# Kernel optimization log

Measured on AMD Instinct MI355X. Metric: run time of the kernel, lower is better.

The kernel has to match this reference:

```python
import jax, jax.numpy as jnp
import numpy as np

N_NODES, N_EDGES = 50000, 800000
IN_DIM, HID, HEADS, OUT_DIM = 256, 32, 8, 16
NEG_SLOPE = 0.2  # PyG GATConv default leaky-relu slope
EPS = 1e-16      # PyG softmax denominator epsilon


def setup_inputs() -> dict:
    key = jax.random.key(0)
    ks = jax.random.split(key, 12)
    x = jax.random.normal(ks[0], (N_NODES, IN_DIM), dtype=jnp.float32)
    edge_index = jax.random.randint(ks[1], (2, N_EDGES), 0, N_NODES, dtype=jnp.int32)
    s1 = 1.0 / np.sqrt(IN_DIM)
    s2 = 1.0 / np.sqrt(HID * HEADS)
    return {
        "x": x,
        "edge_index": edge_index,
        "W1": jax.random.normal(ks[2], (IN_DIM, HEADS * HID), dtype=jnp.float32) * s1,
        "att_src1": jax.random.normal(ks[3], (HEADS, HID), dtype=jnp.float32) * s1,
        "att_dst1": jax.random.normal(ks[4], (HEADS, HID), dtype=jnp.float32) * s1,
        "bias1": jnp.zeros((HEADS * HID,), dtype=jnp.float32),
        "W2": jax.random.normal(ks[5], (HEADS * HID, HEADS * OUT_DIM), dtype=jnp.float32) * s2,
        "att_src2": jax.random.normal(ks[6], (HEADS, OUT_DIM), dtype=jnp.float32) * s2,
        "att_dst2": jax.random.normal(ks[7], (HEADS, OUT_DIM), dtype=jnp.float32) * s2,
        "bias2": jnp.zeros((OUT_DIM,), dtype=jnp.float32),
    }


def _gat_conv(x, src, dst, W, att_src, att_dst, bias, concat):
    # x: [N, F_in]; src/dst: [E'] (self-loops already appended)
    N = x.shape[0]
    H, C = att_src.shape
    h = (x @ W).reshape(N, H, C)                      # [N, H, C]
    a_src = jnp.einsum('nhc,hc->nh', h, att_src)      # [N, H]
    a_dst = jnp.einsum('nhc,hc->nh', h, att_dst)
    e = a_src[src] + a_dst[dst]                       # [E', H]
    e = jax.nn.leaky_relu(e, NEG_SLOPE)
    # segment softmax over edges grouped by destination node
    m = jax.ops.segment_max(e, dst, num_segments=N)   # [N, H]
    e = jnp.exp(e - m[dst])
    denom = jax.ops.segment_sum(e, dst, num_segments=N)
    alpha = e / (denom[dst] + EPS)                    # [E', H]
    msg = h[src] * alpha[:, :, None]                  # [E', H, C] gather+weight
    out = jax.ops.segment_sum(msg, dst, num_segments=N)  # [N, H, C] scatter-add
    if concat:
        out = out.reshape(N, H * C)
    else:
        out = out.mean(axis=1)
    return out + bias


def reference(x, edge_index, W1, att_src1, att_dst1, bias1, W2, att_src2, att_dst2, bias2):
    N = x.shape[0]
    loop = jnp.arange(N, dtype=edge_index.dtype)
    src = jnp.concatenate([edge_index[0], loop])  # PyG add_self_loops=True
    dst = jnp.concatenate([edge_index[1], loop])
    h = _gat_conv(x, src, dst, W1, att_src1, att_dst1, bias1, concat=True)
    h = jax.nn.elu(h)
    out = _gat_conv(h, src, dst, W2, att_src2, att_dst2, bias2, concat=False)
    return out
```

## Files before the change

### kernel.cpp

```cpp
#include <hip/hip_runtime.h>

#define N_NODES 50000
#define N_EDGES 800000
#define EP (N_EDGES + N_NODES)
#define HEADS 8
#define NEG 0.2f

typedef __attribute__((ext_vector_type(8))) short bf16x8;
typedef __attribute__((ext_vector_type(8))) unsigned short u16x8;
typedef __attribute__((ext_vector_type(4))) float f32x4;


__device__ __forceinline__ float bf2f(unsigned short u) {
    return __uint_as_float(((unsigned)u) << 16);
}
__device__ __forceinline__ unsigned short f2bf(float f) {
    unsigned u = __float_as_uint(f);
    return (unsigned short)((u + 0x7FFFu + ((u >> 16) & 1u)) >> 16);
}

__device__ __forceinline__ void get_edge(const int* __restrict__ ei, int e, int& s, int& d) {
    if (e < N_EDGES) { s = ei[e]; d = ei[N_EDGES + e]; }
    else             { s = d = e - N_EDGES; }
}

__device__ __forceinline__ float lrelu(float v) { return v > 0.f ? v : NEG * v; }


#define E_BLOCKS ((EP + 255) / 256)
#define W_ITEMS  (65536 + 32768)
#define W_BLOCKS ((W_ITEMS + 255) / 256)

__global__ void hist_prep(const int* __restrict__ ei, int* __restrict__ cnt,
                          const float* __restrict__ W1, const float* __restrict__ W2,
                          unsigned short* __restrict__ W1T, unsigned short* __restrict__ W2T) {
    const int b = blockIdx.x;
    if (b < E_BLOCKS) {
        int e = b * 256 + threadIdx.x;
        if (e >= EP) return;
        int s, d; get_edge(ei, e, s, d);
        atomicAdd(&cnt[d], 1);
    } else {
        int t = (b - E_BLOCKS) * 256 + threadIdx.x;
        if (t < 65536) {
            int k = t >> 8, n = t & 255;
            W1T[n * 256 + k] = f2bf(W1[k * 256 + n]);
        } else if (t < W_ITEMS) {
            int u = t - 65536; int k = u >> 7, n = u & 127;
            W2T[n * 256 + k] = f2bf(W2[k * 128 + n]);
        }
    }
}


#define SCAN_BLOCKS 196

__global__ __launch_bounds__(256) void scan_p1(const int* __restrict__ cnt,
                                               int* __restrict__ incl, int* __restrict__ bsum) {
    __shared__ int wsum[4];
    const int tid = threadIdx.x, lane = tid & 63, wid = tid >> 6;
    const int idx = blockIdx.x * 256 + tid;
    int v = (idx < N_NODES) ? cnt[idx] : 0;
#pragma unroll
    for (int off = 1; off < 64; off <<= 1) {
        int t = __shfl_up(v, off);
        if (lane >= off) v += t;
    }
    if (lane == 63) wsum[wid] = v;
    __syncthreads();
    int add = 0;
#pragma unroll
    for (int w = 0; w < 4; w++) add += (w < wid) ? wsum[w] : 0;
    incl[idx] = v + add;
    if (tid == 255) bsum[blockIdx.x] = v + add;
}

__global__ __launch_bounds__(256) void scan_p23(const int* __restrict__ incl,
                                                const int* __restrict__ bsum,
                                                int* __restrict__ cnt_cursor,
                                                int* __restrict__ row_start) {
    __shared__ int sb[256];
    __shared__ int wsum[4];
    const int tid = threadIdx.x, lane = tid & 63, wid = tid >> 6;
    int v = (tid < SCAN_BLOCKS) ? bsum[tid] : 0;
#pragma unroll
    for (int off = 1; off < 64; off <<= 1) {
        int t = __shfl_up(v, off);
        if (lane >= off) v += t;
    }
    if (lane == 63) wsum[wid] = v;
    __syncthreads();
    int add = 0;
#pragma unroll
    for (int w = 0; w < 4; w++) add += (w < wid) ? wsum[w] : 0;
    sb[tid] = v + add;
    __syncthreads();
    const int bex = (blockIdx.x == 0) ? 0 : sb[blockIdx.x - 1];
    const int idx = blockIdx.x * 256 + tid;
    if (idx == 0) row_start[N_NODES] = EP;
    if (idx >= N_NODES) return;
    int ex = bex + incl[idx] - cnt_cursor[idx];
    row_start[idx] = ex;
    cnt_cursor[idx] = ex;
}

__global__ void fill_kernel(const int* __restrict__ ei, int* __restrict__ cursor,
                            unsigned short* __restrict__ csr) {
    int e = blockIdx.x * 256 + threadIdx.x;
    if (e >= EP) return;
    int s, d; get_edge(ei, e, s, d);
    int pos = atomicAdd(&cursor[d], 1);
    csr[pos] = (unsigned short)s;
}


template<int NC, int C, bool AF32>
__global__ __launch_bounds__(256) void gemm_fused(const void* __restrict__ Aptr,
        const unsigned short* __restrict__ WT,
        const float* __restrict__ att_s, const float* __restrict__ att_d,
        unsigned short* __restrict__ outh,
        float* __restrict__ a_src, float* __restrict__ a_dst) {
    constexpr int WN  = NC / 4;
    constexpr int NT  = WN / 16;
    constexpr int TPH = C / 16;
    constexpr int BJ  = NC / 32;
    __shared__ unsigned short As[64 * 64];
    __shared__ unsigned short Bs[NC * 64];
    const int m0 = blockIdx.x * 64;
    const int tid  = threadIdx.x;
    const int wave = tid >> 6, lane = tid & 63;
    const int col = lane & 15, quad = lane >> 4;
    const int ar = tid >> 2;
    const int ac = tid & 3;
    const int arow = min(m0 + ar, N_NODES - 1);

    f32x4 acc[4][NT] = {};

    for (int k0 = 0; k0 < 256; k0 += 64) {
        u16x8 av[2];
        if constexpr (AF32) {
            const float* Af = (const float*)Aptr;
#pragma unroll
            for (int j = 0; j < 2; j++) {
                const float* p = Af + (size_t)arow * 256 + k0 + (ac + j * 4) * 8;
                float4 f0 = *(const float4*)p;
                float4 f1 = *(const float4*)(p + 4);
                u16x8 v;
                v[0] = f2bf(f0.x); v[1] = f2bf(f0.y); v[2] = f2bf(f0.z); v[3] = f2bf(f0.w);
                v[4] = f2bf(f1.x); v[5] = f2bf(f1.y); v[6] = f2bf(f1.z); v[7] = f2bf(f1.w);
                av[j] = v;
            }
        } else {
            const unsigned short* Ab = (const unsigned short*)Aptr;
#pragma unroll
            for (int j = 0; j < 2; j++)
                av[j] = *(const u16x8*)(Ab + (size_t)arow * 256 + k0 + (ac + j * 4) * 8);
        }
        u16x8 bv[BJ];
#pragma unroll
        for (int j = 0; j < BJ; j++) {
            int idx = j * 256 + tid, row = idx >> 3, ch = idx & 7;
            bv[j] = *(const u16x8*)(WT + (size_t)row * 256 + k0 + ch * 8);
        }
        __syncthreads();
#pragma unroll
        for (int j = 0; j < 2; j++) {
            int ch = ac + j * 4;
            *(u16x8*)&As[ar * 64 + (ch ^ (ar & 7)) * 8] = av[j];
        }
#pragma unroll
        for (int j = 0; j < BJ; j++) {
            int idx = j * 256 + tid, row = idx >> 3, ch = idx & 7;
            *(u16x8*)&Bs[row * 64 + (ch ^ (row & 7)) * 8] = bv[j];
        }
        __syncthreads();
#pragma unroll
        for (int ks = 0; ks < 64; ks += 32) {
            bf16x8 af[4], bfm[NT];
#pragma unroll
            for (int mi = 0; mi < 4; mi++) {
                int r = mi * 16 + col, c = (ks >> 3) + quad;
                af[mi] = *(const bf16x8*)&As[r * 64 + (c ^ (r & 7)) * 8];
            }
#pragma unroll
            for (int ni = 0; ni < NT; ni++) {
                int r = wave * WN + ni * 16 + col, c = (ks >> 3) + quad;
                bfm[ni] = *(const bf16x8*)&Bs[r * 64 + (c ^ (r & 7)) * 8];
            }
#pragma unroll
            for (int mi = 0; mi < 4; mi++)
#pragma unroll
                for (int ni = 0; ni < NT; ni++)
                    acc[mi][ni] = __builtin_amdgcn_mfma_f32_16x16x32_bf16(
                        af[mi], bfm[ni], acc[mi][ni], 0, 0, 0);
        }
    }

#pragma unroll
    for (int mi = 0; mi < 4; mi++)
#pragma unroll
        for (int ni = 0; ni < NT; ni++)
#pragma unroll
            for (int r = 0; r < 4; r++) {
                int m = m0 + mi * 16 + quad * 4 + r;
                if (m < N_NODES)
                    outh[(size_t)m * NC + wave * WN + ni * 16 + col] = f2bf(acc[mi][ni][r]);
            }

    float asv[NT], adv[NT];
#pragma unroll
    for (int ni = 0; ni < NT; ni++) {
        int n = wave * WN + ni * 16 + col;
        asv[ni] = att_s[n];
        adv[ni] = att_d[n];
    }
#pragma unroll
    for (int mi = 0; mi < 4; mi++)
#pragma unroll
        for (int r = 0; r < 4; r++) {
#pragma unroll
            for (int hl = 0; hl < 2; hl++) {
                float s = 0.f, d = 0.f;
#pragma unroll
                for (int t = 0; t < TPH; t++) {
                    int ni = hl * TPH + t;
                    s = fmaf(acc[mi][ni][r], asv[ni], s);
                    d = fmaf(acc[mi][ni][r], adv[ni], d);
                }
#pragma unroll
                for (int off = 1; off < 16; off <<= 1) {
                    s += __shfl_xor(s, off);
                    d += __shfl_xor(d, off);
                }
                if (col == 0) {
                    int m = m0 + mi * 16 + quad * 4 + r;
                    if (m < N_NODES) {
                        int hh = wave * 2 + hl;
                        a_src[m * 8 + hh] = s;
                        a_dst[m * 8 + hh] = d;
                    }
                }
            }
        }
}


__global__ __launch_bounds__(256) void gat_agg_l1(const int* __restrict__ row_start,
        const unsigned short* __restrict__ csr,
        const unsigned short* __restrict__ hfeat, const float* __restrict__ a_src,
        const float* __restrict__ a_dst, const float* __restrict__ bias,
        unsigned short* __restrict__ outp) {
    const int n    = blockIdx.x * 4 + (threadIdx.x >> 6);
    const int lane = threadIdx.x & 63;
    if (n >= N_NODES) return;

    const int rs  = row_start[n];
    const int deg = row_start[n + 1] - rs;
    const int p   = lane >> 5;
    const int q   = lane & 31;
    const int hq  = q >> 2;
    const float adstf = a_dst[n * 8 + hq];

    float acc[8] = {};
    float den = 0.f;

    for (int c0 = 0; c0 < deg; c0 += 64) {
        const int cnt = min(64, deg - c0);
        int myid = (lane < cnt) ? (int)csr[rs + c0 + lane] : 0;
        int e = 0;
        for (; e + 8 <= cnt; e += 8) {
            int ss[4];
#pragma unroll
            for (int j = 0; j < 4; j++) ss[j] = __shfl(myid, e + j * 2 + p);
            float as[4];
#pragma unroll
            for (int j = 0; j < 4; j++) as[j] = a_src[ss[j] * 8 + hq];
            u16x8 v[4];
#pragma unroll
            for (int j = 0; j < 4; j++)
                v[j] = *(const u16x8*)(hfeat + (size_t)ss[j] * 256 + q * 8);
#pragma unroll
            for (int j = 0; j < 4; j++) {
                float w = __expf(lrelu(as[j] + adstf));
                den += w;
#pragma unroll
                for (int k = 0; k < 8; k++)
                    acc[k] = fmaf(w, bf2f(v[j][k]), acc[k]);
            }
        }
        for (; e < cnt; e += 2) {
            int idx = e + p;
            bool ok = idx < cnt;
            int s = __shfl(myid, ok ? idx : cnt - 1);
            float w = ok ? __expf(lrelu(a_src[s * 8 + hq] + adstf)) : 0.f;
            den += w;
            u16x8 v = *(const u16x8*)(hfeat + (size_t)s * 256 + q * 8);
#pragma unroll
            for (int k = 0; k < 8; k++)
                acc[k] = fmaf(w, bf2f(v[k]), acc[k]);
        }
    }

    den += __shfl_xor(den, 32);
#pragma unroll
    for (int k = 0; k < 8; k++) acc[k] += __shfl_xor(acc[k], 32);

    if (p == 0) {
        const float inv = 1.f / (den + 1e-16f);
        float4 b0 = *(const float4*)(bias + q * 8);
        float4 b1 = *(const float4*)(bias + q * 8 + 4);
        float bb[8] = {b0.x, b0.y, b0.z, b0.w, b1.x, b1.y, b1.z, b1.w};
        u16x8 o;
#pragma unroll
        for (int k = 0; k < 8; k++) {
            float v = acc[k] * inv + bb[k];
            o[k] = f2bf(v > 0.f ? v : __expf(v) - 1.f);
        }
        *(u16x8*)(outp + (size_t)n * 256 + q * 8) = o;
    }
}


__global__ __launch_bounds__(256) void gat_agg_l2(const int* __restrict__ row_start,
        const unsigned short* __restrict__ csr,
        const unsigned short* __restrict__ hfeat, const float* __restrict__ a_src,
        const float* __restrict__ a_dst, const float* __restrict__ bias,
        float* __restrict__ outp) {
    const int n    = blockIdx.x * 4 + (threadIdx.x >> 6);
    const int lane = threadIdx.x & 63;
    if (n >= N_NODES) return;

    const int rs  = row_start[n];
    const int deg = row_start[n + 1] - rs;
    const int hf  = lane >> 3;
    const float adstf = a_dst[n * 8 + hf];

    float acc0 = 0.f, acc1 = 0.f, den = 0.f;

    for (int c0 = 0; c0 < deg; c0 += 64) {
        const int cnt = min(64, deg - c0);
        int myid = (lane < cnt) ? (int)csr[rs + c0 + lane] : 0;
        int e = 0;
        for (; e + 8 <= cnt; e += 8) {
            int ss[8];
#pragma unroll
            for (int j = 0; j < 8; j++) ss[j] = __shfl(myid, e + j);
            float as[8];
#pragma unroll
            for (int j = 0; j < 8; j++) as[j] = a_src[ss[j] * 8 + hf];
            ushort2 v[8];
#pragma unroll
            for (int j = 0; j < 8; j++)
                v[j] = *(const ushort2*)(hfeat + (size_t)ss[j] * 128 + lane * 2);
#pragma unroll
            for (int j = 0; j < 8; j++) {
                float w = __expf(lrelu(as[j] + adstf));
                den += w;
                acc0 = fmaf(w, bf2f(v[j].x), acc0);
                acc1 = fmaf(w, bf2f(v[j].y), acc1);
            }
        }
        for (; e < cnt; e++) {
            int s = __shfl(myid, e);
            float w = __expf(lrelu(a_src[s * 8 + hf] + adstf));
            den += w;
            ushort2 hv = *(const ushort2*)(hfeat + (size_t)s * 128 + lane * 2);
            acc0 = fmaf(w, bf2f(hv.x), acc0);
            acc1 = fmaf(w, bf2f(hv.y), acc1);
        }
    }

    const float inv = 1.f / (den + 1e-16f);
    float a0 = acc0 * inv, a1 = acc1 * inv;
#pragma unroll
    for (int off = 8; off <= 32; off <<= 1) {
        a0 += __shfl_xor(a0, off);
        a1 += __shfl_xor(a1, off);
    }
    if (lane < 8) {
        float2 o;
        o.x = a0 * 0.125f + bias[lane * 2 + 0];
        o.y = a1 * 0.125f + bias[lane * 2 + 1];
        *(float2*)(outp + (size_t)n * 16 + lane * 2) = o;
    }
}


extern "C" void kernel_launch(void* const* d_in, const int* in_sizes, int n_in,
                              void* d_out, int out_size, void* d_ws, size_t ws_size,
                              hipStream_t stream) {
    const float* x        = (const float*)d_in[0];
    const int*   ei       = (const int*)d_in[1];
    const float* W1       = (const float*)d_in[2];
    const float* att_src1 = (const float*)d_in[3];
    const float* att_dst1 = (const float*)d_in[4];
    const float* bias1    = (const float*)d_in[5];
    const float* W2       = (const float*)d_in[6];
    const float* att_src2 = (const float*)d_in[7];
    const float* att_dst2 = (const float*)d_in[8];
    const float* bias2    = (const float*)d_in[9];
    float* out = (float*)d_out;

    char* ws = (char*)d_ws;
    unsigned short* h1  = (unsigned short*)(ws);
    unsigned short* h2  = (unsigned short*)(ws);
    unsigned short* x2b = (unsigned short*)(ws + 32ull * 1024 * 1024);
    unsigned short* W1T = (unsigned short*)(ws + 64ull * 1024 * 1024);
    unsigned short* W2T = W1T + 65536;
    char* aux = ws + 66ull * 1024 * 1024;
    float*          a_src     = (float*)(aux);
    float*          a_dst     = (float*)(aux + 1600000);
    int*            row_start = (int*)  (aux + 3200000);
    int*            cnt       = (int*)  (aux + 3400064);
    unsigned short* csr       = (unsigned short*)(aux + 3600128);
    int*            incl      = (int*)  (aux + 5300128);
    int*            bsum      = (int*)  (aux + 5500832);

    const int MT = (N_NODES + 63) / 64;
    const int AGG_BLOCKS = (N_NODES + 3) / 4;

    hipMemsetAsync(cnt, 0, N_NODES * sizeof(int), stream);
    hist_prep<<<E_BLOCKS + W_BLOCKS, 256, 0, stream>>>(ei, cnt, W1, W2, W1T, W2T);
    scan_p1<<<SCAN_BLOCKS, 256, 0, stream>>>(cnt, incl, bsum);
    scan_p23<<<SCAN_BLOCKS, 256, 0, stream>>>(incl, bsum, cnt, row_start);
    fill_kernel<<<E_BLOCKS, 256, 0, stream>>>(ei, cnt, csr);

    gemm_fused<256, 32, true><<<MT, 256, 0, stream>>>(x, W1T, att_src1, att_dst1, h1, a_src, a_dst);
    gat_agg_l1<<<AGG_BLOCKS, 256, 0, stream>>>(row_start, csr, h1, a_src, a_dst, bias1, x2b);

    gemm_fused<128, 16, false><<<MT, 256, 0, stream>>>(x2b, W2T, att_src2, att_dst2, h2, a_src, a_dst);
    gat_agg_l2<<<AGG_BLOCKS, 256, 0, stream>>>(row_start, csr, h2, a_src, a_dst, bias2, out);
}
```

Baseline: 337.8 us.

## Overlap CSR fill with layer-1 GEMM and fold count zeroing into weight prep

Replaces the memset plus combined hist/weight-prep kernel with a zeroing+weight-transpose kernel followed by a separate histogram kernel. The CSR fill scatter is merged into the layer-1 GEMM launch as extra blocks, so the atomic-heavy fill can run concurrently with the compute-bound GEMM. This removes one memset and lets two independent stages share the GPU, at the cost of a larger combined grid and possible contention between GEMM and atomic blocks.

```diff
diff --git a/kernel.cpp b/kernel.cpp
--- a/kernel.cpp
+++ b/kernel.cpp
@@ -10,6 +10,12 @@
 typedef __attribute__((ext_vector_type(8))) unsigned short u16x8;
 typedef __attribute__((ext_vector_type(4))) float f32x4;
 
+#define E_BLOCKS ((EP + 255) / 256)
+#define MT_BLOCKS ((N_NODES + 63) / 64)
+#define SCAN_BLOCKS 196
+#define W_ITEMS  (65536 + 32768)
+#define W_BLOCKS ((W_ITEMS + 255) / 256)
+
 
 __device__ __forceinline__ float bf2f(unsigned short u) {
     return __uint_as_float(((unsigned)u) << 16);
@@ -27,21 +33,15 @@
 __device__ __forceinline__ float lrelu(float v) { return v > 0.f ? v : NEG * v; }
 
 
-#define E_BLOCKS ((EP + 255) / 256)
-#define W_ITEMS  (65536 + 32768)
-#define W_BLOCKS ((W_ITEMS + 255) / 256)
-
-__global__ void hist_prep(const int* __restrict__ ei, int* __restrict__ cnt,
-                          const float* __restrict__ W1, const float* __restrict__ W2,
-                          unsigned short* __restrict__ W1T, unsigned short* __restrict__ W2T) {
+__global__ void zero_wprep(int* __restrict__ cnt,
+                           const float* __restrict__ W1, const float* __restrict__ W2,
+                           unsigned short* __restrict__ W1T, unsigned short* __restrict__ W2T) {
     const int b = blockIdx.x;
-    if (b < E_BLOCKS) {
-        int e = b * 256 + threadIdx.x;
-        if (e >= EP) return;
-        int s, d; get_edge(ei, e, s, d);
-        atomicAdd(&cnt[d], 1);
+    if (b < SCAN_BLOCKS) {
+        int idx = b * 256 + threadIdx.x;
+        if (idx < N_NODES) cnt[idx] = 0;
     } else {
-        int t = (b - E_BLOCKS) * 256 + threadIdx.x;
+        int t = (b - SCAN_BLOCKS) * 256 + threadIdx.x;
         if (t < 65536) {
             int k = t >> 8, n = t & 255;
             W1T[n * 256 + k] = f2bf(W1[k * 256 + n]);
@@ -53,7 +53,13 @@
 }
 
 
-#define SCAN_BLOCKS 196
+__global__ void hist_kernel(const int* __restrict__ ei, int* __restrict__ cnt) {
+    int e = blockIdx.x * 256 + threadIdx.x;
+    if (e >= EP) return;
+    int s, d; get_edge(ei, e, s, d);
+    atomicAdd(&cnt[d], 1);
+}
+
 
 __global__ __launch_bounds__(256) void scan_p1(const int* __restrict__ cnt,
                                                int* __restrict__ incl, int* __restrict__ bsum) {
@@ -104,18 +110,9 @@
     cnt_cursor[idx] = ex;
 }
 
-__global__ void fill_kernel(const int* __restrict__ ei, int* __restrict__ cursor,
-                            unsigned short* __restrict__ csr) {
-    int e = blockIdx.x * 256 + threadIdx.x;
-    if (e >= EP) return;
-    int s, d; get_edge(ei, e, s, d);
-    int pos = atomicAdd(&cursor[d], 1);
-    csr[pos] = (unsigned short)s;
-}
-
 
 template<int NC, int C, bool AF32>
-__global__ __launch_bounds__(256) void gemm_fused(const void* __restrict__ Aptr,
+__device__ __forceinline__ void gemm_body(int bx, const void* __restrict__ Aptr,
         const unsigned short* __restrict__ WT,
         const float* __restrict__ att_s, const float* __restrict__ att_d,
         unsigned short* __restrict__ outh,
@@ -126,7 +123,7 @@
     constexpr int BJ  = NC / 32;
     __shared__ unsigned short As[64 * 64];
     __shared__ unsigned short Bs[NC * 64];
-    const int m0 = blockIdx.x * 64;
+    const int m0 = bx * 64;
     const int tid  = threadIdx.x;
     const int wave = tid >> 6, lane = tid & 63;
     const int col = lane & 15, quad = lane >> 4;
@@ -242,6 +239,33 @@
                 }
             }
         }
+}
+
+
+__global__ __launch_bounds__(256) void gemm1_fill(const float* __restrict__ x,
+        const unsigned short* __restrict__ W1T,
+        const float* __restrict__ att_s, const float* __restrict__ att_d,
+        unsigned short* __restrict__ outh,
+        float* __restrict__ a_src, float* __restrict__ a_dst,
+        const int* __restrict__ ei, int* __restrict__ cursor,
+        unsigned short* __restrict__ csr) {
+    if (blockIdx.x < MT_BLOCKS) {
+        gemm_body<256, 32, true>(blockIdx.x, x, W1T, att_s, att_d, outh, a_src, a_dst);
+    } else {
+        int e = (blockIdx.x - MT_BLOCKS) * 256 + threadIdx.x;
+        if (e >= EP) return;
+        int s, d; get_edge(ei, e, s, d);
+        int pos = atomicAdd(&cursor[d], 1);
+        csr[pos] = (unsigned short)s;
+    }
+}
+
+__global__ __launch_bounds__(256) void gemm2_kernel(const unsigned short* __restrict__ x2b,
+        const unsigned short* __restrict__ W2T,
+        const float* __restrict__ att_s, const float* __restrict__ att_d,
+        unsigned short* __restrict__ outh,
+        float* __restrict__ a_src, float* __restrict__ a_dst) {
+    gemm_body<128, 16, false>(blockIdx.x, x2b, W2T, att_s, att_d, outh, a_src, a_dst);
 }
 
 
@@ -416,18 +440,17 @@
     int*            incl      = (int*)  (aux + 5300128);
     int*            bsum      = (int*)  (aux + 5500832);
 
-    const int MT = (N_NODES + 63) / 64;
     const int AGG_BLOCKS = (N_NODES + 3) / 4;
 
-    hipMemsetAsync(cnt, 0, N_NODES * sizeof(int), stream);
-    hist_prep<<<E_BLOCKS + W_BLOCKS, 256, 0, stream>>>(ei, cnt, W1, W2, W1T, W2T);
+    zero_wprep<<<SCAN_BLOCKS + W_BLOCKS, 256, 0, stream>>>(cnt, W1, W2, W1T, W2T);
+    hist_kernel<<<E_BLOCKS, 256, 0, stream>>>(ei, cnt);
     scan_p1<<<SCAN_BLOCKS, 256, 0, stream>>>(cnt, incl, bsum);
     scan_p23<<<SCAN_BLOCKS, 256, 0, stream>>>(incl, bsum, cnt, row_start);
-    fill_kernel<<<E_BLOCKS, 256, 0, stream>>>(ei, cnt, csr);
-
-    gemm_fused<256, 32, true><<<MT, 256, 0, stream>>>(x, W1T, att_src1, att_dst1, h1, a_src, a_dst);
+
+    gemm1_fill<<<MT_BLOCKS + E_BLOCKS, 256, 0, stream>>>(x, W1T, att_src1, att_dst1,
+                                                         h1, a_src, a_dst, ei, cnt, csr);
     gat_agg_l1<<<AGG_BLOCKS, 256, 0, stream>>>(row_start, csr, h1, a_src, a_dst, bias1, x2b);
 
-    gemm_fused<128, 16, false><<<MT, 256, 0, stream>>>(x2b, W2T, att_src2, att_dst2, h2, a_src, a_dst);
+    gemm2_kernel<<<MT_BLOCKS, 256, 0, stream>>>(x2b, W2T, att_src2, att_dst2, h2, a_src, a_dst);
     gat_agg_l2<<<AGG_BLOCKS, 256, 0, stream>>>(row_start, csr, h2, a_src, a_dst, bias2, out);
 }
```

After: 333.5 us. About the same (-1.3%).
